# Kernel optimization log

Measured on AMD Instinct MI355X. Metric: run time of the kernel, lower is better.

The kernel has to match this reference:

```python
import jax, jax.numpy as jnp
import numpy as np

LN_EPS = 1e-5
BN_EPS = 1e-5
N_TARGETS = 7


def setup_inputs() -> dict:
    key = jax.random.key(0)
    ks = jax.random.split(key, 12)
    B, N, W, Fin = 64, 40, 256, 64
    H, D = 4, 32
    C = H * D  # gat_out = 128
    L, K = 4, 3  # tcn layers / kernel
    FC = 128
    x = jax.random.normal(ks[0], (B, N, W, Fin), dtype=jnp.float32)
    adj = (jax.random.uniform(ks[1], (N, N)) < 0.3).astype(jnp.float32)
    adj = jnp.maximum(adj, jnp.eye(N, dtype=jnp.float32))  # self-loops
    s = 0.05
    return {
        "x": x,
        "adj": adj,
        "gat_w": jax.random.normal(ks[2], (C, Fin), dtype=jnp.float32) * s,
        "a_src": jax.random.normal(ks[3], (H, D), dtype=jnp.float32) * s,
        "a_dst": jax.random.normal(ks[4], (H, D), dtype=jnp.float32) * s,
        "ln_g": jnp.ones((C,), jnp.float32),
        "ln_b": jnp.zeros((C,), jnp.float32),
        "c1w": jax.random.normal(ks[5], (L, C, C, K), dtype=jnp.float32) * s,
        "c1b": jnp.zeros((L, C), jnp.float32),
        "c2w": jax.random.normal(ks[6], (L, C, C, K), dtype=jnp.float32) * s,
        "c2b": jnp.zeros((L, C), jnp.float32),
        "bn1s": jnp.ones((L, C), jnp.float32),
        "bn1b": jnp.zeros((L, C), jnp.float32),
        "bn1m": jnp.zeros((L, C), jnp.float32),
        "bn1v": jnp.ones((L, C), jnp.float32),
        "bn2s": jnp.ones((L, C), jnp.float32),
        "bn2b": jnp.zeros((L, C), jnp.float32),
        "bn2m": jnp.zeros((L, C), jnp.float32),
        "bn2v": jnp.ones((L, C), jnp.float32),
        "f1w": jax.random.normal(ks[7], (FC, C), dtype=jnp.float32) * s,
        "f1b": jnp.zeros((FC,), jnp.float32),
        "f2w": jax.random.normal(ks[8], (1, FC), dtype=jnp.float32) * s,
        "f2b": jnp.zeros((1,), jnp.float32),
    }


def reference(x, adj, gat_w, a_src, a_dst, ln_g, ln_b,
              c1w, c1b, c2w, c2b,
              bn1s, bn1b, bn1m, bn1v, bn2s, bn2b, bn2m, bn2v,
              f1w, f1b, f2w, f2b):
    B, N, W, Fin = x.shape
    H, D = a_src.shape
    C = H * D
    # --- GAT, vectorized over all W timesteps at once (same math as the per-t loop) ---
    h = jnp.einsum('bnwf,of->bnwo', x, gat_w).reshape(B, N, W, H, D)
    e_src = jnp.einsum('bnwhd,hd->bnwh', h, a_src)  # (B,N,W,H)
    e_dst = jnp.einsum('bnwhd,hd->bnwh', h, a_dst)
    # scores[b,i,w,h,j] = leaky_relu(e_src[b,i] + e_dst[b,j])
    scores = e_src[:, :, :, :, None] + jnp.transpose(e_dst, (0, 2, 3, 1))[:, None]  # (B,N,W,H,N)
    scores = jax.nn.leaky_relu(scores, 0.2)
    mask = adj[None, :, None, None, :] != 0
    scores = jnp.where(mask, scores, -1e9)
    attn = jax.nn.softmax(scores, axis=-1)  # softmax over destination j
    gat = jnp.einsum('bnwhj,bjwhd->bnwhd', attn, h).reshape(B, N, W, C)
    # --- LayerNorm over feature dim ---
    mu = gat.mean(-1, keepdims=True)
    var = gat.var(-1, keepdims=True)
    g = (gat - mu) / jnp.sqrt(var + LN_EPS) * ln_g + ln_b
    # --- TCN over per-node temporal sequences: (B*N, C, W) ---
    seq = jnp.transpose(g.reshape(B * N, W, C), (0, 2, 1))
    K = c1w.shape[-1]

    def bn(z, s, b, m, v):
        return (z - m[None, :, None]) / jnp.sqrt(v[None, :, None] + BN_EPS) * s[None, :, None] + b[None, :, None]

    def cconv(z, w, b, dil):
        pad = (K - 1) * dil  # causal left-padding
        y = jax.lax.conv_general_dilated(z, w, window_strides=(1,), padding=[(pad, 0)],
                                         rhs_dilation=(dil,), dimension_numbers=('NCH', 'OIH', 'NCH'))
        return y + b[None, :, None]

    cur = seq
    for i in range(c1w.shape[0]):  # fixed small number of TCN blocks
        dil = 2 ** i
        o = jax.nn.gelu(bn(cconv(cur, c1w[i], c1b[i], dil), bn1s[i], bn1b[i], bn1m[i], bn1v[i]), approximate=False)
        o = jax.nn.gelu(bn(cconv(o, c2w[i], c2b[i], dil), bn2s[i], bn2b[i], bn2m[i], bn2v[i]), approximate=False)
        cur = jax.nn.gelu(o + cur, approximate=False)  # residual is Identity (in_ch == out_ch)
    h_last = cur[:, :, -1].reshape(B, N, C)
    t = h_last[:, :N_TARGETS, :]  # target_indices = range(7)
    z = jax.nn.gelu(jnp.einsum('bnc,hc->bnh', t, f1w) + f1b, approximate=False)
    logits = (jnp.einsum('bnh,oh->bno', z, f2w) + f2b)[..., 0]  # (B, 7)
    return logits
```

## Files before the change

### kernel.cpp

```cpp
#include <hip/hip_runtime.h>
#include <hip/hip_bf16.h>
#include <math.h>

#define Bb   64
#define Nn   40
#define Ww   256
#define FIN  64
#define Hh   4
#define Dd   32
#define Cc   128
#define NT   7
#define FC   128
#define WT   61
#define W0   195
#define PSTRIDE 520
#define HS2  132

#define XPAN1 512
#define PREPB 193

#define SEQHI_OFF  0u
#define SEQ_BYTES  (448u * WT * Cc * 2u)
#define SEQLO_OFF  (SEQHI_OFF + SEQ_BYTES)
#define WBH_OFF    (SEQLO_OFF + SEQ_BYTES)
#define WB_BYTES   (8u * 4u * 24u * 64u * 8u * 2u)
#define WBL_OFF    (WBH_OFF + WB_BYTES)
#define PSB_OFF    (WBL_OFF + WB_BYTES)
#define PSS_OFF    (PSB_OFF + 4096u)
#define PSH_OFF    (PSS_OFF + 4096u)
#define WPHASE_US  49152u

typedef __attribute__((ext_vector_type(8)))  short short8;
typedef __attribute__((ext_vector_type(16))) float f32x16;

__device__ __forceinline__ float gelu_exact(float v) {
    const float z = v * 0.70710678118654752440f;
    const float a = fabsf(z);
    const float t = 1.0f / fmaf(0.3275911f, a, 1.0f);
    float p = fmaf(t, 1.061405429f, -1.453152027f);
    p = fmaf(t, p, 1.421413741f);
    p = fmaf(t, p, -0.284496736f);
    p = fmaf(t, p, 0.254829592f);
    p *= t;
    const float e = 1.0f - p * __expf(-a * a);
    const float erfv = copysignf(e, z);
    return 0.5f * v * (1.0f + erfv);
}
__device__ __forceinline__ float b2f(ushort u) {
    union { uint i; float f; } c; c.i = ((uint)u) << 16; return c.f;
}
__device__ __forceinline__ void split_bf16(float v, ushort& h, ushort& l) {
    __hip_bfloat16 bh = __float2bfloat16(v);
    float fh = __bfloat162float(bh);
    __hip_bfloat16 bl = __float2bfloat16(v - fh);
    h = *(ushort*)&bh; l = *(ushort*)&bl;
}

__global__ __launch_bounds__(256)
__attribute__((amdgpu_waves_per_eu(4)))
void gat_prep_kernel(
    const float* __restrict__ x, const float* __restrict__ adj,
    const float* __restrict__ gat_w,
    const float* __restrict__ a_src, const float* __restrict__ a_dst,
    const float* __restrict__ ln_g, const float* __restrict__ ln_b,
    const float* __restrict__ c1w, const float* __restrict__ c1b,
    const float* __restrict__ c2w, const float* __restrict__ c2b,
    const float* __restrict__ bn1s, const float* __restrict__ bn1b,
    const float* __restrict__ bn1m, const float* __restrict__ bn1v,
    const float* __restrict__ bn2s, const float* __restrict__ bn2b,
    const float* __restrict__ bn2m, const float* __restrict__ bn2v,
    char* __restrict__ ws,
    ushort* __restrict__ seq_hi, ushort* __restrict__ seq_lo)
{
    __shared__ __align__(16) char pool[2 * 8192];
    __shared__ __align__(16) float h_lds[Nn * HS2];

    const int tid = threadIdx.x;

    if (blockIdx.x < PREPB) {
        if (blockIdx.x < 192) {
            const int t = blockIdx.x * 256 + tid;
            const int lane  = t & 63;
            const int kstep = (t >> 6) % 24;
            const int nt    = ((t >> 6) / 24) & 3;
            const int p     = (t >> 6) / 96;
            const int l = p >> 1, cv = p & 1;
            const int co = nt * 32 + (lane & 31);
            const float* wsrc = cv ? c2w : c1w;
            ushort* wbh = (ushort*)(ws + WBH_OFF);
            ushort* wbl = (ushort*)(ws + WBL_OFF);
#pragma unroll
            for (int j = 0; j < 8; ++j) {
                const int k  = kstep * 16 + ((lane >> 5) << 3) + j;
                const int kk = k >> 7, ci = k & 127;
                const float w = wsrc[((size_t)(l * Cc + co) * Cc + ci) * 3 + kk];
                ushort h, lo; split_bf16(w, h, lo);
                wbh[(size_t)t * 8 + j] = h;
                wbl[(size_t)t * 8 + j] = lo;
            }
        } else {
            float* psb = (float*)(ws + PSB_OFF);
            float* pss = (float*)(ws + PSS_OFF);
            float* psh = (float*)(ws + PSH_OFF);
            for (int idx = tid; idx < 1024; idx += 256) {
                const int p = idx >> 7, co = idx & 127;
                const int l = p >> 1, cv = p & 1;
                const int lc = l * Cc + co;
                const float s  = cv ? bn2s[lc] : bn1s[lc];
                const float bb = cv ? bn2b[lc] : bn1b[lc];
                const float m  = cv ? bn2m[lc] : bn1m[lc];
                const float vv = cv ? bn2v[lc] : bn1v[lc];
                const float cb = cv ? c2b[lc] : c1b[lc];
                const float scale = s * rsqrtf(vv + 1e-5f);
                pss[idx] = scale;
                psh[idx] = bb - m * scale;
                psb[idx] = cb;
            }
        }
        return;
    }

    ushort* xa_hi = (ushort*)pool;
    ushort* xa_lo = (ushort*)(pool + 8192);
    float* e_lds    = (float*)pool;
    float* attn_lds = (float*)(pool + 1280);
    float* g_lds    = (float*)(pool + 5760);

    const int blk = blockIdx.x - PREPB;
    const int b   = blk / WT;
    const int tau = blk % WT;
    const int w   = W0 + tau;

    for (int idx = tid; idx < Nn * 8; idx += 256) {
        const int n  = idx >> 3;
        const int oc = idx & 7;
        const float* src = x + ((size_t)(b * Nn + n) * Ww + w) * FIN + oc * 8;
        const float4 f0 = *(const float4*)(src);
        const float4 f1 = *(const float4*)(src + 4);
        ushort h[8], l[8];
        split_bf16(f0.x, h[0], l[0]); split_bf16(f0.y, h[1], l[1]);
        split_bf16(f0.z, h[2], l[2]); split_bf16(f0.w, h[3], l[3]);
        split_bf16(f1.x, h[4], l[4]); split_bf16(f1.y, h[5], l[5]);
        split_bf16(f1.z, h[6], l[6]); split_bf16(f1.w, h[7], l[7]);
        const int dst = oc * XPAN1 + n * 8;
        *(uint4*)(xa_hi + dst) = *(uint4*)h;
        *(uint4*)(xa_lo + dst) = *(uint4*)l;
    }
    __syncthreads();

    {
        const int wave = tid >> 6;
        const int lane = tid & 63;
        const int nt   = wave;
        const int q2   = lane >> 5;
        const int m32  = lane & 31;
        const int co   = nt * 32 + m32;

        short8 BH[4], BL[4];
#pragma unroll
        for (int ks = 0; ks < 4; ++ks) {
            const float* gp = gat_w + co * FIN + ks * 16 + q2 * 8;
            const float4 f0 = *(const float4*)(gp);
            const float4 f1 = *(const float4*)(gp + 4);
            ushort h[8], l[8];
            split_bf16(f0.x, h[0], l[0]); split_bf16(f0.y, h[1], l[1]);
            split_bf16(f0.z, h[2], l[2]); split_bf16(f0.w, h[3], l[3]);
            split_bf16(f1.x, h[4], l[4]); split_bf16(f1.y, h[5], l[5]);
            split_bf16(f1.z, h[6], l[6]); split_bf16(f1.w, h[7], l[7]);
            BH[ks] = *(short8*)h;
            BL[ks] = *(short8*)l;
        }

#pragma unroll
        for (int mt = 0; mt < 2; ++mt) {
            f32x16 acc;
#pragma unroll
            for (int i = 0; i < 16; ++i) acc[i] = 0.f;
#pragma unroll
            for (int ks = 0; ks < 4; ++ks) {
                const int aoff = (ks * 2 + q2) * XPAN1 + (mt * 32 + m32) * 8;
                const short8 ah = *(const short8*)(xa_hi + aoff);
                const short8 al = *(const short8*)(xa_lo + aoff);
                acc = __builtin_amdgcn_mfma_f32_32x32x16_bf16(ah, BH[ks], acc, 0, 0, 0);
                acc = __builtin_amdgcn_mfma_f32_32x32x16_bf16(al, BH[ks], acc, 0, 0, 0);
                acc = __builtin_amdgcn_mfma_f32_32x32x16_bf16(ah, BL[ks], acc, 0, 0, 0);
            }
#pragma unroll
            for (int reg = 0; reg < 16; ++reg) {
                const int row = mt * 32 + (reg & 3) + 8 * (reg >> 2) + 4 * q2;
                if (row < Nn) h_lds[row * HS2 + co] = acc[reg];
            }
        }
    }
    __syncthreads();

    for (int u = tid; u < 2 * Nn * Hh; u += 256) {
        const int s  = u & 1;
        const int hh = (u >> 1) & 3;
        const int n  = u >> 3;
        const float* av = (s ? a_dst : a_src) + hh * Dd;
        const float* hp = h_lds + n * HS2 + hh * Dd;
        float acc = 0.f;
#pragma unroll
        for (int i = 0; i < 8; ++i) {
            const float4 hv = *(const float4*)(hp + i * 4);
            const float4 avv = *(const float4*)(av + i * 4);
            acc += hv.x * avv.x + hv.y * avv.y + hv.z * avv.z + hv.w * avv.w;
        }
        e_lds[s * (Nn * Hh) + n * Hh + hh] = acc;
    }
    __syncthreads();

    if (tid < NT * Hh) {
        const int n  = tid >> 2;
        const int hh = tid & 3;
        const float es = e_lds[n * Hh + hh];
        float sc[Nn];
        float mx = -1e30f;
#pragma unroll
        for (int j = 0; j < Nn; ++j) {
            float s = es + e_lds[Nn * Hh + j * Hh + hh];
            s = (s > 0.f) ? s : 0.2f * s;
            if (adj[n * Nn + j] == 0.0f) s = -1e9f;
            sc[j] = s;
            mx = fmaxf(mx, s);
        }
        float sum = 0.f;
#pragma unroll
        for (int j = 0; j < Nn; ++j) { const float p = expf(sc[j] - mx); sc[j] = p; sum += p; }
        const float inv = 1.0f / sum;
#pragma unroll
        for (int j = 0; j < Nn; ++j)
            attn_lds[(n * Hh + hh) * Nn + j] = sc[j] * inv;
    }
    __syncthreads();

    if (tid < NT * 32) {
        const int n    = tid >> 5;
        const int cq   = tid & 31;
        const int c0   = cq * 4;
        const int head = cq >> 3;
        const float* ap = attn_lds + (n * Hh + head) * Nn;
        float4 acc = make_float4(0.f, 0.f, 0.f, 0.f);
        for (int j = 0; j < Nn; ++j) {
            const float a = ap[j];
            const float4 hv = *(const float4*)(h_lds + j * HS2 + c0);
            acc.x += a * hv.x; acc.y += a * hv.y;
            acc.z += a * hv.z; acc.w += a * hv.w;
        }
        *(float4*)(g_lds + n * Cc + c0) = acc;
    }
    __syncthreads();

    if (tid < NT * 32) {
        const int n = tid >> 5, lane = tid & 31;
        const float4 v = ((const float4*)(g_lds + n * Cc))[lane];
        float s  = v.x + v.y + v.z + v.w;
        float sq = v.x*v.x + v.y*v.y + v.z*v.z + v.w*v.w;
#pragma unroll
        for (int off = 16; off; off >>= 1) {
            s  += __shfl_xor(s, off, 32);
            sq += __shfl_xor(sq, off, 32);
        }
        const float mu   = s * (1.0f / Cc);
        const float rstd = rsqrtf(sq * (1.0f / Cc) - mu * mu + 1e-5f);
        const float4 gg = ((const float4*)ln_g)[lane];
        const float4 bb = ((const float4*)ln_b)[lane];
        float o0 = (v.x - mu) * rstd * gg.x + bb.x;
        float o1 = (v.y - mu) * rstd * gg.y + bb.y;
        float o2 = (v.z - mu) * rstd * gg.z + bb.z;
        float o3 = (v.w - mu) * rstd * gg.w + bb.w;
        const int r = b * NT + n;
        ushort4 uh, ul;
        split_bf16(o0, uh.x, ul.x);
        split_bf16(o1, uh.y, ul.y);
        split_bf16(o2, uh.z, ul.z);
        split_bf16(o3, uh.w, ul.w);
        const int p  = (lane >> 2) * 2 + ((lane >> 1) & 1);
        const int j0 = (lane & 1) * 4;
        const size_t off = ((size_t)(r * 16 + p) * WT + tau) * 8 + j0;
        *(ushort4*)(seq_hi + off) = uh;
        *(ushort4*)(seq_lo + off) = ul;
    }
}

__device__ __forceinline__ void conv_sk(
    const ushort* in_hi, const ushort* in_lo,
    ushort* out_hi, ushort* out_lo,
    float* scratch,
    const ushort* __restrict__ wbh, const ushort* __restrict__ wbl,
    const float* __restrict__ psb, const float* __restrict__ pss,
    const float* __restrict__ psh,
    const int tau0, const int d, const int kh, const int nt,
    const int lane, const bool residual)
{
    const int m  = lane & 31;
    const int q2 = lane >> 5;
    const bool skipA = (tau0 > 31);

    int rA0a = m - 2 * d; rA0a = rA0a < 0 ? 0 : rA0a;
    int rA1a = m - d;     rA1a = rA1a < 0 ? 0 : rA1a;
    const int rA2a = m;
    const int rA0b = 32 + m - 2 * d;
    const int rA1b = 32 + m - d;
    const int rA2b = 32 + m;

    const ushort* wb_h = wbh + (size_t)(nt * 24 + kh * 12) * 512 + lane * 8;
    const ushort* wb_l = wbl + (size_t)(nt * 24 + kh * 12) * 512 + lane * 8;

    const int co = nt * 32 + m;
    const float bsv = psb[co], scv = pss[co], shv = psh[co];
    const int colb = ((co >> 4) * 2 + ((co >> 3) & 1)) * PSTRIDE + (co & 7);

    f32x16 accA, accB;
#pragma unroll
    for (int i = 0; i < 16; ++i) { accA[i] = 0.f; accB[i] = 0.f; }

    short8 WH[4], WL[4];
#pragma unroll
    for (int i = 0; i < 4; ++i) {
        WH[i] = *(const short8*)(wb_h + i * 512);
        WL[i] = *(const short8*)(wb_l + i * 512);
    }

#pragma unroll
    for (int i = 0; i < 12; ++i) {
        const int slot = i & 3;
        const short8 bh = WH[slot];
        const short8 bl = WL[slot];
        if (i + 4 < 12) {
            WH[slot] = *(const short8*)(wb_h + (i + 4) * 512);
            WL[slot] = *(const short8*)(wb_l + (i + 4) * 512);
        }
        const int ks = kh * 12 + i;
        const int kk = ks >> 3;
        const int panel = (((ks & 7) << 1) + q2) * PSTRIDE;
        if (!skipA) {
            const int ra = (kk == 0) ? rA0a : (kk == 1 ? rA1a : rA2a);
            const short8 ahA = *(const short8*)(in_hi + panel + ra * 8);
            const short8 alA = *(const short8*)(in_lo + panel + ra * 8);
            accA = __builtin_amdgcn_mfma_f32_32x32x16_bf16(ahA, bh, accA, 0, 0, 0);
            accA = __builtin_amdgcn_mfma_f32_32x32x16_bf16(alA, bh, accA, 0, 0, 0);
            accA = __builtin_amdgcn_mfma_f32_32x32x16_bf16(ahA, bl, accA, 0, 0, 0);
        }
        {
            const int rb = (kk == 0) ? rA0b : (kk == 1 ? rA1b : rA2b);
            const short8 ahB = *(const short8*)(in_hi + panel + rb * 8);
            const short8 alB = *(const short8*)(in_lo + panel + rb * 8);
            accB = __builtin_amdgcn_mfma_f32_32x32x16_bf16(ahB, bh, accB, 0, 0, 0);
            accB = __builtin_amdgcn_mfma_f32_32x32x16_bf16(alB, bh, accB, 0, 0, 0);
            accB = __builtin_amdgcn_mfma_f32_32x32x16_bf16(ahB, bl, accB, 0, 0, 0);
        }
    }

    if (residual) __syncthreads();

    if (kh == 0) {
        float* dst = scratch + ((4 + nt) << 10) + lane;
#pragma unroll
        for (int r = 0; r < 16; ++r) dst[r * 64] = accB[r];
    } else if (!skipA) {
        float* dst = scratch + (nt << 10) + lane;
#pragma unroll
        for (int r = 0; r < 16; ++r) dst[r * 64] = accA[r];
    }
    __syncthreads();

    f32x16 acc;
    if (kh == 0) {
        acc = accA;
        if (!skipA) {
            const float* srcp = scratch + (nt << 10) + lane;
#pragma unroll
            for (int r = 0; r < 16; ++r) acc[r] += srcp[r * 64];
        }
    } else {
        acc = accB;
        const float* srcp = scratch + ((4 + nt) << 10) + lane;
#pragma unroll
        for (int r = 0; r < 16; ++r) acc[r] += srcp[r * 64];
    }

    if (!residual) __syncthreads();

    if (!(skipA && kh == 0)) {
        const int mt = kh;
#pragma unroll
        for (int reg = 0; reg < 16; ++reg) {
            const int row = (reg & 3) + 8 * (reg >> 2) + 4 * q2;
            const int tau = mt * 32 + row;
            if (tau >= tau0 && tau <= 60) {
                float v = (acc[reg] + bsv) * scv + shv;
                v = gelu_exact(v);
                const int off = colb + tau * 8;
                if (residual)
                    v = gelu_exact(v + b2f(out_hi[off]) + b2f(out_lo[off]));
                ushort uh, ul; split_bf16(v, uh, ul);
                out_hi[off] = uh; out_lo[off] = ul;
            }
        }
    }
}

__global__ __launch_bounds__(512)
__attribute__((amdgpu_waves_per_eu(4)))
void tcn_head_kernel(
    const char* __restrict__ ws,
    const float* __restrict__ f1w, const float* __restrict__ f1b,
    const float* __restrict__ f2w, const float* __restrict__ f2b,
    float* __restrict__ out)
{
    __shared__ __align__(16) ushort cur_hi[16 * PSTRIDE];
    __shared__ __align__(16) ushort cur_lo[16 * PSTRIDE];
    __shared__ __align__(16) ushort o1_pair[2][16 * PSTRIDE];
    __shared__ float red[FC];

    ushort* o1_hi = o1_pair[0];
    ushort* o1_lo = o1_pair[1];
    float*  scratch = (float*)o1_pair;

    const int tid = threadIdx.x;
    const int r   = blockIdx.x;

    const ushort* seq_hi = (const ushort*)(ws + SEQHI_OFF);
    const ushort* seq_lo = (const ushort*)(ws + SEQLO_OFF);
    const ushort* WBH    = (const ushort*)(ws + WBH_OFF);
    const ushort* WBL    = (const ushort*)(ws + WBL_OFF);
    const float*  PSB    = (const float*)(ws + PSB_OFF);
    const float*  PSS    = (const float*)(ws + PSS_OFF);
    const float*  PSH    = (const float*)(ws + PSH_OFF);

    {
        const size_t base = (size_t)r * (16 * WT * 8);
        for (int i = tid; i < 16 * WT; i += 512) {
            const int p = i / WT, row = i - p * WT;
            const int dst = p * PSTRIDE + row * 8;
            *(uint4*)(cur_hi + dst) = *(const uint4*)(seq_hi + base + i * 8);
            *(uint4*)(cur_lo + dst) = *(const uint4*)(seq_lo + base + i * 8);
        }
    }
    __syncthreads();

    const int wave = tid >> 6;
    const int lane = tid & 63;
    const int nt   = wave & 3;
    const int kh   = wave >> 2;

    const int tau0_1[4] = {2, 8, 20, 44};
    const int tau0_2[4] = {4, 12, 28, 60};

#pragma unroll
    for (int l = 0; l < 4; ++l) {
        const int d  = 1 << l;
        const int p1 = 2 * l, p2 = 2 * l + 1;
        conv_sk(cur_hi, cur_lo, o1_hi, o1_lo, scratch,
                WBH + (size_t)p1 * WPHASE_US, WBL + (size_t)p1 * WPHASE_US,
                PSB + p1 * Cc, PSS + p1 * Cc, PSH + p1 * Cc,
                tau0_1[l], d, kh, nt, lane, false);
        __syncthreads();
        conv_sk(o1_hi, o1_lo, cur_hi, cur_lo, scratch,
                WBH + (size_t)p2 * WPHASE_US, WBL + (size_t)p2 * WPHASE_US,
                PSB + p2 * Cc, PSS + p2 * Cc, PSH + p2 * Cc,
                tau0_2[l], d, kh, nt, lane, true);
        __syncthreads();
    }

    if (tid < FC) {
        const float4* wr = (const float4*)(f1w + tid * Cc);
        float acc = 0.f;
#pragma unroll
        for (int i = 0; i < Cc / 4; ++i) {
            const float4 wv = wr[i];
            const int ci0 = i * 4;
            const int off = ((ci0 >> 4) * 2 + ((ci0 >> 3) & 1)) * PSTRIDE
                          + 60 * 8 + (ci0 & 7);
            const ushort4 vh = *(const ushort4*)(cur_hi + off);
            const ushort4 vl = *(const ushort4*)(cur_lo + off);
            acc += wv.x * (b2f(vh.x) + b2f(vl.x))
                 + wv.y * (b2f(vh.y) + b2f(vl.y))
                 + wv.z * (b2f(vh.z) + b2f(vl.z))
                 + wv.w * (b2f(vh.w) + b2f(vl.w));
        }
        red[tid] = gelu_exact(acc + f1b[tid]) * f2w[tid];
    }
    __syncthreads();
    if (tid < 64) {
        float v = red[tid] + red[tid + 64];
#pragma unroll
        for (int off = 32; off; off >>= 1) v += __shfl_xor(v, off, 64);
        if (tid == 0) out[r] = v + f2b[0];
    }
}

extern "C" void kernel_launch(void* const* d_in, const int* in_sizes, int n_in,
                              void* d_out, int out_size, void* d_ws, size_t ws_size,
                              hipStream_t stream) {
    const float* x     = (const float*)d_in[0];
    const float* adj   = (const float*)d_in[1];
    const float* gat_w = (const float*)d_in[2];
    const float* a_src = (const float*)d_in[3];
    const float* a_dst = (const float*)d_in[4];
    const float* ln_g  = (const float*)d_in[5];
    const float* ln_b  = (const float*)d_in[6];
    const float* c1w   = (const float*)d_in[7];
    const float* c1b   = (const float*)d_in[8];
    const float* c2w   = (const float*)d_in[9];
    const float* c2b   = (const float*)d_in[10];
    const float* bn1s  = (const float*)d_in[11];
    const float* bn1b  = (const float*)d_in[12];
    const float* bn1m  = (const float*)d_in[13];
    const float* bn1v  = (const float*)d_in[14];
    const float* bn2s  = (const float*)d_in[15];
    const float* bn2b  = (const float*)d_in[16];
    const float* bn2m  = (const float*)d_in[17];
    const float* bn2v  = (const float*)d_in[18];
    const float* f1w   = (const float*)d_in[19];
    const float* f1b   = (const float*)d_in[20];
    const float* f2w   = (const float*)d_in[21];
    const float* f2b   = (const float*)d_in[22];

    char* ws = (char*)d_ws;

    gat_prep_kernel<<<PREPB + Bb * WT, 256, 0, stream>>>(
        x, adj, gat_w, a_src, a_dst, ln_g, ln_b,
        c1w, c1b, c2w, c2b,
        bn1s, bn1b, bn1m, bn1v, bn2s, bn2b, bn2m, bn2v,
        ws, (ushort*)(ws + SEQHI_OFF), (ushort*)(ws + SEQLO_OFF));

    tcn_head_kernel<<<Bb * NT, 512, 0, stream>>>(
        ws, f1w, f1b, f2w, f2b, (float*)d_out);
}
```

Measured before the change: 367.1 us.

## Split TCN conv work by output time tile instead of K halves

The conv work split across the 8 waves changes from split-K (each wave computes half the reduction for both M tiles, then reduces through shared scratch) to split-M (each wave owns one 32-row time tile and the full 24-step K loop). This drops the scratch reduction and its extra barriers. Waves whose tile lies entirely before tau0 now return early, and the weight prefetch is deepened to 6 slots. The three-product MFMA chain is spread across two accumulators for more instruction-level parallelism. The catch is load imbalance: in deep layers only the second M-tile waves do any work, each running twice as many K steps.

Result: slower. 383.7 us (+4.5%).

```diff
diff --git a/kernel.cpp b/kernel.cpp
--- a/kernel.cpp
+++ b/kernel.cpp
@@ -284,120 +284,90 @@
     }
 }
 
-__device__ __forceinline__ void conv_sk(
+__device__ __forceinline__ void conv_mfma(
     const ushort* in_hi, const ushort* in_lo,
     ushort* out_hi, ushort* out_lo,
-    float* scratch,
     const ushort* __restrict__ wbh, const ushort* __restrict__ wbl,
     const float* __restrict__ psb, const float* __restrict__ pss,
     const float* __restrict__ psh,
-    const int tau0, const int d, const int kh, const int nt,
+    const int tau0, const int d, const int mt, const int nt,
     const int lane, const bool residual)
 {
+    if (mt * 32 + 31 < tau0) return;
+
     const int m  = lane & 31;
     const int q2 = lane >> 5;
-    const bool skipA = (tau0 > 31);
-
-    int rA0a = m - 2 * d; rA0a = rA0a < 0 ? 0 : rA0a;
-    int rA1a = m - d;     rA1a = rA1a < 0 ? 0 : rA1a;
-    const int rA2a = m;
-    const int rA0b = 32 + m - 2 * d;
-    const int rA1b = 32 + m - d;
-    const int rA2b = 32 + m;
-
-    const ushort* wb_h = wbh + (size_t)(nt * 24 + kh * 12) * 512 + lane * 8;
-    const ushort* wb_l = wbl + (size_t)(nt * 24 + kh * 12) * 512 + lane * 8;
-
     const int co = nt * 32 + m;
+    const int mbase = mt * 32 + m;
+
     const float bsv = psb[co], scv = pss[co], shv = psh[co];
     const int colb = ((co >> 4) * 2 + ((co >> 3) & 1)) * PSTRIDE + (co & 7);
 
-    f32x16 accA, accB;
-#pragma unroll
-    for (int i = 0; i < 16; ++i) { accA[i] = 0.f; accB[i] = 0.f; }
-
-    short8 WH[4], WL[4];
-#pragma unroll
-    for (int i = 0; i < 4; ++i) {
-        WH[i] = *(const short8*)(wb_h + i * 512);
-        WL[i] = *(const short8*)(wb_l + i * 512);
-    }
-
-#pragma unroll
-    for (int i = 0; i < 12; ++i) {
-        const int slot = i & 3;
-        const short8 bh = WH[slot];
-        const short8 bl = WL[slot];
-        if (i + 4 < 12) {
-            WH[slot] = *(const short8*)(wb_h + (i + 4) * 512);
-            WL[slot] = *(const short8*)(wb_l + (i + 4) * 512);
-        }
-        const int ks = kh * 12 + i;
-        const int kk = ks >> 3;
-        const int panel = (((ks & 7) << 1) + q2) * PSTRIDE;
-        if (!skipA) {
-            const int ra = (kk == 0) ? rA0a : (kk == 1 ? rA1a : rA2a);
-            const short8 ahA = *(const short8*)(in_hi + panel + ra * 8);
-            const short8 alA = *(const short8*)(in_lo + panel + ra * 8);
-            accA = __builtin_amdgcn_mfma_f32_32x32x16_bf16(ahA, bh, accA, 0, 0, 0);
-            accA = __builtin_amdgcn_mfma_f32_32x32x16_bf16(alA, bh, accA, 0, 0, 0);
-            accA = __builtin_amdgcn_mfma_f32_32x32x16_bf16(ahA, bl, accA, 0, 0, 0);
-        }
-        {
-            const int rb = (kk == 0) ? rA0b : (kk == 1 ? rA1b : rA2b);
-            const short8 ahB = *(const short8*)(in_hi + panel + rb * 8);
-            const short8 alB = *(const short8*)(in_lo + panel + rb * 8);
-            accB = __builtin_amdgcn_mfma_f32_32x32x16_bf16(ahB, bh, accB, 0, 0, 0);
-            accB = __builtin_amdgcn_mfma_f32_32x32x16_bf16(alB, bh, accB, 0, 0, 0);
-            accB = __builtin_amdgcn_mfma_f32_32x32x16_bf16(ahB, bl, accB, 0, 0, 0);
-        }
-    }
-
-    if (residual) __syncthreads();
-
-    if (kh == 0) {
-        float* dst = scratch + ((4 + nt) << 10) + lane;
-#pragma unroll
-        for (int r = 0; r < 16; ++r) dst[r * 64] = accB[r];
-    } else if (!skipA) {
-        float* dst = scratch + (nt << 10) + lane;
-#pragma unroll
-        for (int r = 0; r < 16; ++r) dst[r * 64] = accA[r];
-    }
-    __syncthreads();
-
-    f32x16 acc;
-    if (kh == 0) {
-        acc = accA;
-        if (!skipA) {
-            const float* srcp = scratch + (nt << 10) + lane;
-#pragma unroll
-            for (int r = 0; r < 16; ++r) acc[r] += srcp[r * 64];
-        }
-    } else {
-        acc = accB;
-        const float* srcp = scratch + ((4 + nt) << 10) + lane;
-#pragma unroll
-        for (int r = 0; r < 16; ++r) acc[r] += srcp[r * 64];
-    }
-
-    if (!residual) __syncthreads();
-
-    if (!(skipA && kh == 0)) {
-        const int mt = kh;
+    float rc[16];
+    if (residual) {
 #pragma unroll
         for (int reg = 0; reg < 16; ++reg) {
             const int row = (reg & 3) + 8 * (reg >> 2) + 4 * q2;
             const int tau = mt * 32 + row;
-            if (tau >= tau0 && tau <= 60) {
-                float v = (acc[reg] + bsv) * scv + shv;
-                v = gelu_exact(v);
-                const int off = colb + tau * 8;
-                if (residual)
-                    v = gelu_exact(v + b2f(out_hi[off]) + b2f(out_lo[off]));
-                ushort uh, ul; split_bf16(v, uh, ul);
-                out_hi[off] = uh; out_lo[off] = ul;
-            }
+            const int off = colb + tau * 8;
+            rc[reg] = (tau >= tau0 && tau <= 60)
+                    ? (b2f(out_hi[off]) + b2f(out_lo[off])) : 0.f;
+        }
+    }
+
+    int rA0 = mbase - 2 * d; rA0 = rA0 < 0 ? 0 : rA0;
+    int rA1 = mbase - d;     rA1 = rA1 < 0 ? 0 : rA1;
+    const int rA2 = mbase;
+
+    const ushort* wb_h = wbh + (size_t)(nt * 24) * 512 + lane * 8;
+    const ushort* wb_l = wbl + (size_t)(nt * 24) * 512 + lane * 8;
+
+    f32x16 acc0, acc1;
+#pragma unroll
+    for (int i = 0; i < 16; ++i) { acc0[i] = 0.f; acc1[i] = 0.f; }
+
+    short8 WH[6], WL[6];
+#pragma unroll
+    for (int i = 0; i < 6; ++i) {
+        WH[i] = *(const short8*)(wb_h + i * 512);
+        WL[i] = *(const short8*)(wb_l + i * 512);
+    }
+
+#pragma unroll
+    for (int ks = 0; ks < 24; ++ks) {
+        const int slot = ks % 6;
+        const short8 bh = WH[slot];
+        const short8 bl = WL[slot];
+        if (ks + 6 < 24) {
+            WH[slot] = *(const short8*)(wb_h + (ks + 6) * 512);
+            WL[slot] = *(const short8*)(wb_l + (ks + 6) * 512);
+        }
+        const int kk   = ks >> 3;
+        const int rowA = (kk == 0) ? rA0 : (kk == 1 ? rA1 : rA2);
+        const int aoff = (((ks & 7) << 1) + q2) * PSTRIDE + rowA * 8;
+        const short8 ah = *(const short8*)(in_hi + aoff);
+        const short8 al = *(const short8*)(in_lo + aoff);
+        acc0 = __builtin_amdgcn_mfma_f32_32x32x16_bf16(ah, bh, acc0, 0, 0, 0);
+        acc1 = __builtin_amdgcn_mfma_f32_32x32x16_bf16(al, bh, acc1, 0, 0, 0);
+        if (ks & 1)
+            acc0 = __builtin_amdgcn_mfma_f32_32x32x16_bf16(ah, bl, acc0, 0, 0, 0);
+        else
+            acc1 = __builtin_amdgcn_mfma_f32_32x32x16_bf16(ah, bl, acc1, 0, 0, 0);
+    }
+#pragma unroll
+    for (int i = 0; i < 16; ++i) acc0[i] += acc1[i];
+
+#pragma unroll
+    for (int reg = 0; reg < 16; ++reg) {
+        const int row = (reg & 3) + 8 * (reg >> 2) + 4 * q2;
+        const int tau = mt * 32 + row;
+        if (tau >= tau0 && tau <= 60) {
+            float v = (acc0[reg] + bsv) * scv + shv;
+            v = gelu_exact(v);
+            if (residual) v = gelu_exact(v + rc[reg]);
+            ushort uh, ul; split_bf16(v, uh, ul);
+            const int off = colb + tau * 8;
+            out_hi[off] = uh; out_lo[off] = ul;
         }
     }
 }
@@ -412,12 +382,9 @@
 {
     __shared__ __align__(16) ushort cur_hi[16 * PSTRIDE];
     __shared__ __align__(16) ushort cur_lo[16 * PSTRIDE];
-    __shared__ __align__(16) ushort o1_pair[2][16 * PSTRIDE];
+    __shared__ __align__(16) ushort o1_hi [16 * PSTRIDE];
+    __shared__ __align__(16) ushort o1_lo [16 * PSTRIDE];
     __shared__ float red[FC];
-
-    ushort* o1_hi = o1_pair[0];
-    ushort* o1_lo = o1_pair[1];
-    float*  scratch = (float*)o1_pair;
 
     const int tid = threadIdx.x;
     const int r   = blockIdx.x;
@@ -444,7 +411,7 @@
     const int wave = tid >> 6;
     const int lane = tid & 63;
     const int nt   = wave & 3;
-    const int kh   = wave >> 2;
+    const int mt   = wave >> 2;
 
     const int tau0_1[4] = {2, 8, 20, 44};
     const int tau0_2[4] = {4, 12, 28, 60};
@@ -453,15 +420,15 @@
     for (int l = 0; l < 4; ++l) {
         const int d  = 1 << l;
         const int p1 = 2 * l, p2 = 2 * l + 1;
-        conv_sk(cur_hi, cur_lo, o1_hi, o1_lo, scratch,
-                WBH + (size_t)p1 * WPHASE_US, WBL + (size_t)p1 * WPHASE_US,
-                PSB + p1 * Cc, PSS + p1 * Cc, PSH + p1 * Cc,
-                tau0_1[l], d, kh, nt, lane, false);
+        conv_mfma(cur_hi, cur_lo, o1_hi, o1_lo,
+                  WBH + (size_t)p1 * WPHASE_US, WBL + (size_t)p1 * WPHASE_US,
+                  PSB + p1 * Cc, PSS + p1 * Cc, PSH + p1 * Cc,
+                  tau0_1[l], d, mt, nt, lane, false);
         __syncthreads();
-        conv_sk(o1_hi, o1_lo, cur_hi, cur_lo, scratch,
-                WBH + (size_t)p2 * WPHASE_US, WBL + (size_t)p2 * WPHASE_US,
-                PSB + p2 * Cc, PSS + p2 * Cc, PSH + p2 * Cc,
-                tau0_2[l], d, kh, nt, lane, true);
+        conv_mfma(o1_hi, o1_lo, cur_hi, cur_lo,
+                  WBH + (size_t)p2 * WPHASE_US, WBL + (size_t)p2 * WPHASE_US,
+                  PSB + p2 * Cc, PSS + p2 * Cc, PSH + p2 * Cc,
+                  tau0_2[l], d, mt, nt, lane, true);
         __syncthreads();
     }
 
```
